# Performance work log

Measured on AMD Instinct MI355X. Metric: run time of the kernel, lower is better.

The kernel has to match this reference:

```python
import jax, jax.numpy as jnp
import numpy as np

DIM = 512
NUM_HEADS = 8
HEAD_SIZE = 64
INNER = NUM_HEADS * HEAD_SIZE  # 512


def setup_inputs() -> dict:
    key = jax.random.key(0)
    k1, k2, k3, k4, k5 = jax.random.split(key, 5)
    x = jax.random.normal(k1, (2, 4096, DIM), dtype=jnp.float32)
    # Linear params stored as [in, out] for y = x @ W + b (same math as torch Linear)
    w_qkv = jax.random.normal(k2, (DIM, INNER * 3), dtype=jnp.float32) * (1.0 / np.sqrt(DIM))
    b_qkv = jax.random.normal(k3, (INNER * 3,), dtype=jnp.float32) * 0.01
    w_out = jax.random.normal(k4, (INNER, DIM), dtype=jnp.float32) * (1.0 / np.sqrt(INNER))
    b_out = jax.random.normal(k5, (DIM,), dtype=jnp.float32) * 0.01
    return {"x": x, "w_qkv": w_qkv, "b_qkv": b_qkv, "w_out": w_out, "b_out": b_out}


def reference(x, w_qkv, b_qkv, w_out, b_out):
    b, n, _ = x.shape
    qkv = x @ w_qkv + b_qkv                      # [b, n, 3*inner]
    q, k, v = jnp.split(qkv, 3, axis=-1)          # each [b, n, inner]

    def heads(t):  # 'b n (h d) -> b h n d'
        return t.reshape(b, n, NUM_HEADS, HEAD_SIZE).transpose(0, 2, 1, 3)

    q, k, v = heads(q), heads(k), heads(v)
    scores = jnp.einsum('bhnd,bhmd->bhnm', q, k) / jnp.sqrt(jnp.float32(HEAD_SIZE))
    probs = jax.nn.softmax(scores, axis=-1)       # dropout is identity in eval
    out = jnp.einsum('bhnm,bhmd->bhnd', probs, v)
    out = out.transpose(0, 2, 1, 3).reshape(b, n, INNER)  # 'b h n d -> b n (h d)'
    return out @ w_out + b_out
```

## Files before the change

kernel.cpp:

```cpp
#include <hip/hip_runtime.h>

typedef __bf16 bf16;
typedef __bf16 bf16x8 __attribute__((ext_vector_type(8)));
typedef float f32x4 __attribute__((ext_vector_type(4)));

#define MFMA16(a, b, c) __builtin_amdgcn_mfma_f32_16x16x32_bf16((a), (b), (c), 0, 0, 0)

static __device__ __forceinline__ bf16x8 ldg8(const bf16* p) {
  return *(const bf16x8*)p;
}


__global__ __launch_bounds__(256) void cvt_pack_x(const float* __restrict__ x,
                                                  bf16* __restrict__ Xp) {
  int mt = blockIdx.x, kc = blockIdx.y;
  int row = threadIdx.x >> 4;
  int c4 = (threadIdx.x & 15) * 4;
  bf16* tile = Xp + ((size_t)mt * 8 + kc) * 4096;
#pragma unroll
  for (int i = 0; i < 4; i++) {
    int r = i * 16 + row;
    const float* src = x + (size_t)(mt * 64 + r) * 512 + kc * 64 + c4;
    float4 v = *(const float4*)src;
    bf16* d = tile + r * 64 + c4;
    d[0] = (bf16)v.x; d[1] = (bf16)v.y; d[2] = (bf16)v.z; d[3] = (bf16)v.w;
  }
}

__global__ __launch_bounds__(256) void transpose_pack_w(const float* __restrict__ W,
                                                        bf16* __restrict__ Wp,
                                                        int N, int KC) {
  __shared__ bf16 tile[64][65];
  int kc = blockIdx.x, nt = blockIdx.y;
  int c = threadIdx.x & 63;
  int r4 = threadIdx.x >> 6;
#pragma unroll
  for (int i = 0; i < 16; i++) {
    int r = r4 * 16 + i;
    tile[r][c] = (bf16)W[(size_t)(kc * 64 + r) * N + nt * 64 + c];
  }
  __syncthreads();
  bf16* dst = Wp + ((size_t)nt * KC + kc) * 4096;
#pragma unroll
  for (int i = 0; i < 16; i++) {
    int r = r4 * 16 + i;
    dst[r * 64 + c] = tile[c][r];
  }
}

__device__ __forceinline__ void gemm_core_packed(const bf16* __restrict__ Ap,
                                                 const bf16* __restrict__ Bp,
                                                 int KC, bf16* Atile, bf16* Btile,
                                                 int tid, int wave, int l16,
                                                 int quad, f32x4 acc[4]) {
  for (int kc = 0; kc < KC; kc++) {
    __syncthreads();
    const bf16* ag = Ap + (size_t)kc * 4096;
    const bf16* bg = Bp + (size_t)kc * 4096;
#pragma unroll
    for (int rnd = 0; rnd < 2; rnd++) {
      int e = (rnd * 256 + tid) * 8;
      int row = e >> 6;
      int c16 = (e & 63) >> 3;
      int unit = row * 8 + (c16 ^ (row & 7));
      *(bf16x8*)&Atile[unit * 8] = ldg8(ag + e);
      *(bf16x8*)&Btile[unit * 8] = ldg8(bg + e);
    }
    __syncthreads();

    int ar = wave * 16 + l16;
    bf16x8 a0 = *(const bf16x8*)&Atile[(ar * 8 + (quad ^ (ar & 7))) * 8];
    bf16x8 a1 = *(const bf16x8*)&Atile[(ar * 8 + ((4 + quad) ^ (ar & 7))) * 8];
#pragma unroll
    for (int ct = 0; ct < 4; ct++) {
      int n = ct * 16 + l16;
      bf16x8 b0 = *(const bf16x8*)&Btile[(n * 8 + (quad ^ (n & 7))) * 8];
      bf16x8 b1 = *(const bf16x8*)&Btile[(n * 8 + ((4 + quad) ^ (n & 7))) * 8];
      acc[ct] = MFMA16(a0, b0, acc[ct]);
      acc[ct] = MFMA16(a1, b1, acc[ct]);
    }
  }
}

__global__ __launch_bounds__(256) void qkv_gemm(const bf16* __restrict__ Xp,
                                                const bf16* __restrict__ Wp1,
                                                const float* __restrict__ bqkv,
                                                bf16* __restrict__ Q,
                                                bf16* __restrict__ Kh,
                                                bf16* __restrict__ Vt) {
  int mt = blockIdx.x, nt = blockIdx.y;
  int tid = threadIdx.x;
  int wave = tid >> 6, lane = tid & 63;
  int l16 = lane & 15, quad = lane >> 4;

  __shared__ __align__(16) bf16 Atile[4096];
  __shared__ __align__(16) bf16 Btile[4096];

  f32x4 acc[4] = {};
  gemm_core_packed(Xp + (size_t)mt * 8 * 4096, Wp1 + (size_t)nt * 8 * 4096, 8,
                   Atile, Btile, tid, wave, l16, quad, acc);

#pragma unroll
  for (int ct = 0; ct < 4; ct++) {
    int c = nt * 64 + ct * 16 + l16;
    float bias = bqkv[c];
    int which = c >> 9, inner = c & 511;
    int h = inner >> 6, d = inner & 63;
#pragma unroll
    for (int r = 0; r < 4; r++) {
      int m = mt * 64 + wave * 16 + quad * 4 + r;
      int b = m >> 12, n = m & 4095;
      int bh = b * 8 + h;
      float v = acc[ct][r] + bias;
      if (which == 0)
        Q[((size_t)bh * 4096 + n) * 64 + d] = (bf16)(v * 0.125f);
      else if (which == 1)
        Kh[((size_t)bh * 4096 + n) * 64 + d] = (bf16)v;
      else
        Vt[(((size_t)bh * 64 + (n >> 6)) * 64 + d) * 64 + (n & 63)] = (bf16)v;
    }
  }
}

__global__ __launch_bounds__(256, 4) void flash_partial(const bf16* __restrict__ Q,
                                                        const bf16* __restrict__ K,
                                                        const bf16* __restrict__ Vt,
                                                        bf16* __restrict__ Opart,
                                                        float* __restrict__ Lpart) {
  int strip = blockIdx.x, bh = blockIdx.y, half = blockIdx.z;
  int tid = threadIdx.x;
  int wave = tid >> 6, lane = tid & 63;
  int l16 = lane & 15, quad = lane >> 4;

  const bf16* Qh = Q + (size_t)bh * 4096 * 64;
  const bf16* Kg = K + ((size_t)bh * 4096 + half * 2048) * 64;
  const bf16* Vg = Vt + (size_t)bh * 64 * 4096 + (size_t)half * 2048 * 64;

  __shared__ __align__(16) bf16 Klds[4096];
  __shared__ __align__(16) bf16 Vlds[4096];
  __shared__ __align__(16) bf16 P[4][32][72];

  int qbase = strip * 128 + wave * 32;
  bf16x8 aq[2][2];
#pragma unroll
  for (int mt = 0; mt < 2; mt++) {
    const bf16* qr = Qh + (size_t)(qbase + mt * 16 + l16) * 64;
    aq[mt][0] = ldg8(qr + quad * 8);
    aq[mt][1] = ldg8(qr + 32 + quad * 8);
  }

  f32x4 o[2][4] = {};
  float l_lane[2][4] = {};

  int e0 = tid * 8, e1 = (256 + tid) * 8;
  int r0 = e0 >> 6, r1 = e1 >> 6;
  int u0 = r0 * 8 + (((e0 & 63) >> 3) ^ (r0 & 7));
  int u1 = r1 * 8 + (((e1 & 63) >> 3) ^ (r1 & 7));

  bf16x8 kp0 = ldg8(Kg + e0), kp1 = ldg8(Kg + e1);
  bf16x8 vp0 = ldg8(Vg + e0), vp1 = ldg8(Vg + e1);

  for (int kb = 0; kb < 2048; kb += 64) {
    __syncthreads();
    *(bf16x8*)&Klds[u0 * 8] = kp0;
    *(bf16x8*)&Klds[u1 * 8] = kp1;
    *(bf16x8*)&Vlds[u0 * 8] = vp0;
    *(bf16x8*)&Vlds[u1 * 8] = vp1;
    __syncthreads();

    if (kb + 64 < 2048) {
      const bf16* kg = Kg + (size_t)(kb + 64) * 64;
      const bf16* vg = Vg + (size_t)(kb + 64) * 64;
      kp0 = ldg8(kg + e0);
      kp1 = ldg8(kg + e1);
      vp0 = ldg8(vg + e0);
      vp1 = ldg8(vg + e1);
    }

    f32x4 s[2][4] = {};
#pragma unroll
    for (int ct = 0; ct < 4; ct++) {
      int n = ct * 16 + l16;
      bf16x8 b0 = *(const bf16x8*)&Klds[(n * 8 + (quad ^ (n & 7))) * 8];
      bf16x8 b1 = *(const bf16x8*)&Klds[(n * 8 + ((4 + quad) ^ (n & 7))) * 8];
#pragma unroll
      for (int mt = 0; mt < 2; mt++) {
        s[mt][ct] = MFMA16(aq[mt][0], b0, s[mt][ct]);
        s[mt][ct] = MFMA16(aq[mt][1], b1, s[mt][ct]);
      }
    }
#pragma unroll
    for (int mt = 0; mt < 2; mt++)
#pragma unroll
      for (int ct = 0; ct < 4; ct++)
#pragma unroll
        for (int r = 0; r < 4; r++) {
          float p = __expf(s[mt][ct][r]);
          l_lane[mt][r] += p;
          P[wave][mt * 16 + quad * 4 + r][ct * 16 + l16] = (bf16)p;
        }
#pragma unroll
    for (int mt = 0; mt < 2; mt++) {
      bf16x8 ap0 = ldg8(&P[wave][mt * 16 + l16][quad * 8]);
      bf16x8 ap1 = ldg8(&P[wave][mt * 16 + l16][32 + quad * 8]);
#pragma unroll
      for (int ct = 0; ct < 4; ct++) {
        int d = ct * 16 + l16;
        bf16x8 bv0 = *(const bf16x8*)&Vlds[(d * 8 + (quad ^ (d & 7))) * 8];
        bf16x8 bv1 = *(const bf16x8*)&Vlds[(d * 8 + ((4 + quad) ^ (d & 7))) * 8];
        o[mt][ct] = MFMA16(ap0, bv0, o[mt][ct]);
        o[mt][ct] = MFMA16(ap1, bv1, o[mt][ct]);
      }
    }
  }

  size_t u = ((size_t)half * 16 + bh) * 32 + strip;
  bf16* op = Opart + u * 8192;
#pragma unroll
  for (int mt = 0; mt < 2; mt++) {
    float lrow[4];
#pragma unroll
    for (int r = 0; r < 4; r++) {
      float l = l_lane[mt][r];
#pragma unroll
      for (int off = 1; off < 16; off <<= 1) l += __shfl_xor(l, off);
      lrow[r] = l;
    }
#pragma unroll
    for (int ct = 0; ct < 4; ct++)
#pragma unroll
      for (int r = 0; r < 4; r++)
        op[(wave * 32 + mt * 16 + quad * 4 + r) * 64 + ct * 16 + l16] =
            (bf16)o[mt][ct][r];
    if (l16 == 0) {
#pragma unroll
      for (int r = 0; r < 4; r++)
        Lpart[u * 128 + wave * 32 + mt * 16 + quad * 4 + r] = lrow[r];
    }
  }
}

__global__ __launch_bounds__(256) void flash_combine(const bf16* __restrict__ Opart,
                                                     const float* __restrict__ Lpart,
                                                     bf16* __restrict__ Ap) {
  int qt = blockIdx.x, bh = blockIdx.y;
  int col = threadIdx.x & 63;
  int rg = threadIdx.x >> 6;
  int strip = qt >> 1;
  int rbase = (qt & 1) * 64;
  size_t u0 = (size_t)bh * 32 + strip;
  size_t u1 = ((size_t)16 + bh) * 32 + strip;
  int b = bh >> 3, h = bh & 7;
  bf16* apt = Ap + (((size_t)(b * 64 + qt)) * 8 + h) * 4096;
#pragma unroll
  for (int i = 0; i < 16; i++) {
    int r64 = rg * 16 + i;
    int row = rbase + r64;
    float o0 = (float)Opart[u0 * 8192 + row * 64 + col];
    float o1 = (float)Opart[u1 * 8192 + row * 64 + col];
    float ls = Lpart[u0 * 128 + row] + Lpart[u1 * 128 + row];
    apt[r64 * 64 + col] = (bf16)((o0 + o1) / ls);
  }
}

__global__ __launch_bounds__(256) void out_gemm(const bf16* __restrict__ Ap,
                                                const bf16* __restrict__ Wp2,
                                                const float* __restrict__ bout,
                                                float* __restrict__ Out) {
  int mt = blockIdx.x, nt = blockIdx.y;
  int tid = threadIdx.x;
  int wave = tid >> 6, lane = tid & 63;
  int l16 = lane & 15, quad = lane >> 4;

  __shared__ __align__(16) bf16 Atile[4096];
  __shared__ __align__(16) bf16 Btile[4096];

  f32x4 acc[4] = {};
  gemm_core_packed(Ap + (size_t)mt * 8 * 4096, Wp2 + (size_t)nt * 8 * 4096, 8,
                   Atile, Btile, tid, wave, l16, quad, acc);

#pragma unroll
  for (int ct = 0; ct < 4; ct++) {
    int c = nt * 64 + ct * 16 + l16;
    float bias = bout[c];
#pragma unroll
    for (int r = 0; r < 4; r++) {
      int m = mt * 64 + wave * 16 + quad * 4 + r;
      Out[(size_t)m * 512 + c] = acc[ct][r] + bias;
    }
  }
}

extern "C" void kernel_launch(void* const* d_in, const int* in_sizes, int n_in,
                              void* d_out, int out_size, void* d_ws,
                              size_t ws_size, hipStream_t stream) {
  const float* x = (const float*)d_in[0];
  const float* w_qkv = (const float*)d_in[1];
  const float* b_qkv = (const float*)d_in[2];
  const float* w_out = (const float*)d_in[3];
  const float* b_out = (const float*)d_in[4];
  float* out = (float*)d_out;

  char* ws = (char*)d_ws;
  bf16* Q = (bf16*)(ws + 0);
  bf16* K = (bf16*)(ws + 8388608);
  bf16* Vt = (bf16*)(ws + 16777216);
  bf16* Ap = (bf16*)(ws + 25165824);
  bf16* Wp1 = (bf16*)(ws + 33554432);
  bf16* Wp2 = (bf16*)(ws + 35127296);
  bf16* Xp = (bf16*)(ws + 35651584);
  bf16* Opart = (bf16*)(ws + 44040192);
  float* Lpart = (float*)(ws + 60817408);

  cvt_pack_x<<<dim3(128, 8), 256, 0, stream>>>(x, Xp);
  transpose_pack_w<<<dim3(8, 24), 256, 0, stream>>>(w_qkv, Wp1, 1536, 8);
  transpose_pack_w<<<dim3(8, 8), 256, 0, stream>>>(w_out, Wp2, 512, 8);
  qkv_gemm<<<dim3(128, 24), 256, 0, stream>>>(Xp, Wp1, b_qkv, Q, K, Vt);
  flash_partial<<<dim3(32, 16, 2), 256, 0, stream>>>(Q, K, Vt, Opart, Lpart);
  flash_combine<<<dim3(64, 16), 256, 0, stream>>>(Opart, Lpart, Ap);
  out_gemm<<<dim3(128, 8), 256, 0, stream>>>(Ap, Wp2, b_out, out);
}
```

Measured before the change: 217.3 us.

## Prefetch GEMM tiles in registers and process two KV tiles per barrier

The packed GEMM core now loads the next K-chunk into registers while the current chunk is computed, so global loads overlap with MFMA work. The flash attention kernel stages two 64-key K/V tiles per sync round and prefetches the next pair. This halves the number of barriers per key range. The cost is more LDS and registers, and the occupancy hint drops from 4 to 3 blocks per CU.

```diff
diff --git a/kernel.cpp b/kernel.cpp
--- a/kernel.cpp
+++ b/kernel.cpp
@@ -53,20 +53,30 @@
                                                  int KC, bf16* Atile, bf16* Btile,
                                                  int tid, int wave, int l16,
                                                  int quad, f32x4 acc[4]) {
+  int e0 = tid * 8, e1 = (256 + tid) * 8;
+  int r0 = e0 >> 6, r1 = e1 >> 6;
+  int u0 = r0 * 8 + (((e0 & 63) >> 3) ^ (r0 & 7));
+  int u1 = r1 * 8 + (((e1 & 63) >> 3) ^ (r1 & 7));
+
+  bf16x8 pa0 = ldg8(Ap + e0), pa1 = ldg8(Ap + e1);
+  bf16x8 pb0 = ldg8(Bp + e0), pb1 = ldg8(Bp + e1);
+
   for (int kc = 0; kc < KC; kc++) {
     __syncthreads();
-    const bf16* ag = Ap + (size_t)kc * 4096;
-    const bf16* bg = Bp + (size_t)kc * 4096;
-#pragma unroll
-    for (int rnd = 0; rnd < 2; rnd++) {
-      int e = (rnd * 256 + tid) * 8;
-      int row = e >> 6;
-      int c16 = (e & 63) >> 3;
-      int unit = row * 8 + (c16 ^ (row & 7));
-      *(bf16x8*)&Atile[unit * 8] = ldg8(ag + e);
-      *(bf16x8*)&Btile[unit * 8] = ldg8(bg + e);
-    }
+    *(bf16x8*)&Atile[u0 * 8] = pa0;
+    *(bf16x8*)&Atile[u1 * 8] = pa1;
+    *(bf16x8*)&Btile[u0 * 8] = pb0;
+    *(bf16x8*)&Btile[u1 * 8] = pb1;
     __syncthreads();
+
+    if (kc + 1 < KC) {
+      const bf16* ag = Ap + (size_t)(kc + 1) * 4096;
+      const bf16* bg = Bp + (size_t)(kc + 1) * 4096;
+      pa0 = ldg8(ag + e0);
+      pa1 = ldg8(ag + e1);
+      pb0 = ldg8(bg + e0);
+      pb1 = ldg8(bg + e1);
+    }
 
     int ar = wave * 16 + l16;
     bf16x8 a0 = *(const bf16x8*)&Atile[(ar * 8 + (quad ^ (ar & 7))) * 8];
@@ -122,7 +132,7 @@
   }
 }
 
-__global__ __launch_bounds__(256, 4) void flash_partial(const bf16* __restrict__ Q,
+__global__ __launch_bounds__(256, 3) void flash_partial(const bf16* __restrict__ Q,
                                                         const bf16* __restrict__ K,
                                                         const bf16* __restrict__ Vt,
                                                         bf16* __restrict__ Opart,
@@ -136,8 +146,8 @@
   const bf16* Kg = K + ((size_t)bh * 4096 + half * 2048) * 64;
   const bf16* Vg = Vt + (size_t)bh * 64 * 4096 + (size_t)half * 2048 * 64;
 
-  __shared__ __align__(16) bf16 Klds[4096];
-  __shared__ __align__(16) bf16 Vlds[4096];
+  __shared__ __align__(16) bf16 Klds[2][4096];
+  __shared__ __align__(16) bf16 Vlds[2][4096];
   __shared__ __align__(16) bf16 P[4][32][72];
 
   int qbase = strip * 128 + wave * 32;
@@ -157,59 +167,76 @@
   int u0 = r0 * 8 + (((e0 & 63) >> 3) ^ (r0 & 7));
   int u1 = r1 * 8 + (((e1 & 63) >> 3) ^ (r1 & 7));
 
-  bf16x8 kp0 = ldg8(Kg + e0), kp1 = ldg8(Kg + e1);
-  bf16x8 vp0 = ldg8(Vg + e0), vp1 = ldg8(Vg + e1);
-
-  for (int kb = 0; kb < 2048; kb += 64) {
+  bf16x8 kp[2][2], vp[2][2];
+#pragma unroll
+  for (int t = 0; t < 2; t++) {
+    const bf16* kg = Kg + (size_t)t * 4096;
+    const bf16* vg = Vg + (size_t)t * 4096;
+    kp[t][0] = ldg8(kg + e0);
+    kp[t][1] = ldg8(kg + e1);
+    vp[t][0] = ldg8(vg + e0);
+    vp[t][1] = ldg8(vg + e1);
+  }
+
+  for (int kb = 0; kb < 2048; kb += 128) {
     __syncthreads();
-    *(bf16x8*)&Klds[u0 * 8] = kp0;
-    *(bf16x8*)&Klds[u1 * 8] = kp1;
-    *(bf16x8*)&Vlds[u0 * 8] = vp0;
-    *(bf16x8*)&Vlds[u1 * 8] = vp1;
+#pragma unroll
+    for (int t = 0; t < 2; t++) {
+      *(bf16x8*)&Klds[t][u0 * 8] = kp[t][0];
+      *(bf16x8*)&Klds[t][u1 * 8] = kp[t][1];
+      *(bf16x8*)&Vlds[t][u0 * 8] = vp[t][0];
+      *(bf16x8*)&Vlds[t][u1 * 8] = vp[t][1];
+    }
     __syncthreads();
 
-    if (kb + 64 < 2048) {
-      const bf16* kg = Kg + (size_t)(kb + 64) * 64;
-      const bf16* vg = Vg + (size_t)(kb + 64) * 64;
-      kp0 = ldg8(kg + e0);
-      kp1 = ldg8(kg + e1);
-      vp0 = ldg8(vg + e0);
-      vp1 = ldg8(vg + e1);
-    }
-
-    f32x4 s[2][4] = {};
-#pragma unroll
-    for (int ct = 0; ct < 4; ct++) {
-      int n = ct * 16 + l16;
-      bf16x8 b0 = *(const bf16x8*)&Klds[(n * 8 + (quad ^ (n & 7))) * 8];
-      bf16x8 b1 = *(const bf16x8*)&Klds[(n * 8 + ((4 + quad) ^ (n & 7))) * 8];
+    if (kb + 128 < 2048) {
+#pragma unroll
+      for (int t = 0; t < 2; t++) {
+        const bf16* kg = Kg + (size_t)(kb + 128 + t * 64) * 64;
+        const bf16* vg = Vg + (size_t)(kb + 128 + t * 64) * 64;
+        kp[t][0] = ldg8(kg + e0);
+        kp[t][1] = ldg8(kg + e1);
+        vp[t][0] = ldg8(vg + e0);
+        vp[t][1] = ldg8(vg + e1);
+      }
+    }
+
+#pragma unroll
+    for (int t = 0; t < 2; t++) {
+      f32x4 s[2][4] = {};
+#pragma unroll
+      for (int ct = 0; ct < 4; ct++) {
+        int n = ct * 16 + l16;
+        bf16x8 b0 = *(const bf16x8*)&Klds[t][(n * 8 + (quad ^ (n & 7))) * 8];
+        bf16x8 b1 = *(const bf16x8*)&Klds[t][(n * 8 + ((4 + quad) ^ (n & 7))) * 8];
+#pragma unroll
+        for (int mt = 0; mt < 2; mt++) {
+          s[mt][ct] = MFMA16(aq[mt][0], b0, s[mt][ct]);
+          s[mt][ct] = MFMA16(aq[mt][1], b1, s[mt][ct]);
+        }
+      }
+#pragma unroll
+      for (int mt = 0; mt < 2; mt++)
+#pragma unroll
+        for (int ct = 0; ct < 4; ct++)
+#pragma unroll
+          for (int r = 0; r < 4; r++) {
+            float p = __expf(s[mt][ct][r]);
+            l_lane[mt][r] += p;
+            P[wave][mt * 16 + quad * 4 + r][ct * 16 + l16] = (bf16)p;
+          }
 #pragma unroll
       for (int mt = 0; mt < 2; mt++) {
-        s[mt][ct] = MFMA16(aq[mt][0], b0, s[mt][ct]);
-        s[mt][ct] = MFMA16(aq[mt][1], b1, s[mt][ct]);
-      }
-    }
-#pragma unroll
-    for (int mt = 0; mt < 2; mt++)
-#pragma unroll
-      for (int ct = 0; ct < 4; ct++)
-#pragma unroll
-        for (int r = 0; r < 4; r++) {
-          float p = __expf(s[mt][ct][r]);
-          l_lane[mt][r] += p;
-          P[wave][mt * 16 + quad * 4 + r][ct * 16 + l16] = (bf16)p;
+        bf16x8 ap0 = ldg8(&P[wave][mt * 16 + l16][quad * 8]);
+        bf16x8 ap1 = ldg8(&P[wave][mt * 16 + l16][32 + quad * 8]);
+#pragma unroll
+        for (int ct = 0; ct < 4; ct++) {
+          int d = ct * 16 + l16;
+          bf16x8 bv0 = *(const bf16x8*)&Vlds[t][(d * 8 + (quad ^ (d & 7))) * 8];
+          bf16x8 bv1 = *(const bf16x8*)&Vlds[t][(d * 8 + ((4 + quad) ^ (d & 7))) * 8];
+          o[mt][ct] = MFMA16(ap0, bv0, o[mt][ct]);
+          o[mt][ct] = MFMA16(ap1, bv1, o[mt][ct]);
         }
-#pragma unroll
-    for (int mt = 0; mt < 2; mt++) {
-      bf16x8 ap0 = ldg8(&P[wave][mt * 16 + l16][quad * 8]);
-      bf16x8 ap1 = ldg8(&P[wave][mt * 16 + l16][32 + quad * 8]);
-#pragma unroll
-      for (int ct = 0; ct < 4; ct++) {
-        int d = ct * 16 + l16;
-        bf16x8 bv0 = *(const bf16x8*)&Vlds[(d * 8 + (quad ^ (d & 7))) * 8];
-        bf16x8 bv1 = *(const bf16x8*)&Vlds[(d * 8 + ((4 + quad) ^ (d & 7))) * 8];
-        o[mt][ct] = MFMA16(ap0, bv0, o[mt][ct]);
-        o[mt][ct] = MFMA16(ap1, bv1, o[mt][ct]);
       }
     }
   }
```

After: 232.6 us. 1.07x slower.
